# Optimization experiments

Hardware: AMD Instinct MI355X
Metric: run time of the kernel (lower is better)

Reference implementation:

```python
import jax, jax.numpy as jnp
import numpy as np

M, K, N, GROUP = 64, 4096, 11008, 128
NGROUPS = K // GROUP  # 32


def setup_inputs() -> dict:
    key = jax.random.key(0)
    k1, k2, k3, k4, k5 = jax.random.split(key, 5)
    x = jax.random.normal(k1, (M, K), dtype=jnp.float32)
    # packed int4 weights: 8 nibbles per int32, full 32-bit entropy
    qweight = jax.random.bits(k2, (K // 8, N), dtype=jnp.uint32).astype(jnp.int32)
    qzeros = jax.random.bits(k3, (NGROUPS, N // 8), dtype=jnp.uint32).astype(jnp.int32)
    scales = jax.random.uniform(k4, (NGROUPS, N), dtype=jnp.float32, minval=0.001, maxval=0.02)
    bias = jax.random.normal(k5, (N,), dtype=jnp.float32) * 0.01
    return {"x": x, "qweight": qweight, "qzeros": qzeros, "scales": scales, "bias": bias}


def dequantize(qweight, qzeros, scales):
    shifts = jnp.arange(8, dtype=jnp.int32) * 4  # nibble bit offsets 0..28
    # unpack weights: [K//8, N] -> [K//8, 8, N] -> [NGROUPS, GROUP, N]
    w = (jnp.right_shift(qweight[:, None, :], shifts[None, :, None]) & 15)
    w = w.reshape(-1, GROUP, qweight.shape[1])
    # unpack zeros: [NGROUPS, N//8] -> [NGROUPS, N//8, 8] -> [NGROUPS, 1, N]; GPTQ stores zero-1
    z = (jnp.right_shift(qzeros[:, :, None], shifts[None, None, :]) & 15) + 1
    z = z.reshape(z.shape[0], 1, -1)
    # scale * (q - zero), per group: [NGROUPS, GROUP, N] -> [K, N]
    W = scales[:, None, :] * (w - z).astype(scales.dtype)
    return W.reshape(-1, W.shape[2])


def reference(x, qweight, qzeros, scales, bias):
    W = dequantize(qweight, qzeros, scales)  # [K, N] fp32
    return jnp.matmul(x, W.astype(x.dtype)) + bias
```

## Files before the change

kernel.cpp:

```cpp
#include <hip/hip_runtime.h>
#include <hip/hip_bf16.h>

namespace {

constexpr int MM = 64;
constexpr int KK = 4096;
constexpr int NN = 11008;
constexpr int NZROW = NN / 8;
constexpr int BN = 128;
constexpr int KSPLIT = 8;
constexpr int KSEG = KK / KSPLIT;
constexpr int NTILES = NN / BN;
constexpr int SCK = 128;
constexpr int NSC = KSEG / SCK;
constexpr int AROW = 68;
constexpr int ABUF = MM * AROW;
constexpr size_t WS_NEED = (size_t)KSPLIT * MM * NN * 4;

typedef float f32x4 __attribute__((ext_vector_type(4)));
typedef short s16x8 __attribute__((ext_vector_type(8)));
typedef int   i32x4 __attribute__((ext_vector_type(4)));

__device__ __forceinline__ int perm_trunc(float even, float odd) {
  return (int)__builtin_amdgcn_perm(__float_as_uint(odd), __float_as_uint(even), 0x07060302u);
}
__device__ __forceinline__ unsigned rne_adj(float f) {
  unsigned u = __float_as_uint(f);
  return u + 0x7FFFu + ((u >> 16) & 1u);
}
__device__ __forceinline__ int pack_rne(float even, float odd) {
  return (int)__builtin_amdgcn_perm(rne_adj(odd), rne_adj(even), 0x07060302u);
}

__global__ __launch_bounds__(256) void prep_kernel(
    const float* __restrict__ bias, float* __restrict__ out)
{
  const int i = blockIdx.x * 256 + threadIdx.x;
  out[i] = bias[i % NN];
}

__global__ __launch_bounds__(256) void reduce_kernel(
    const float* __restrict__ ws, const float* __restrict__ bias,
    float* __restrict__ out)
{
  const int i4 = (blockIdx.x * 256 + threadIdx.x) * 4;
  f32x4 acc = *(const f32x4*)(bias + (i4 % NN));
  #pragma unroll
  for (int s = 0; s < KSPLIT; ++s)
    acc += *(const f32x4*)(ws + (size_t)s * (MM * NN) + i4);
  *(f32x4*)(out + i4) = acc;
}

template<bool ATOMIC>
__global__ __launch_bounds__(256, 3) void gptq_gemm_kernel(
    const float* __restrict__ x, const int* __restrict__ qw,
    const int* __restrict__ qz, const float* __restrict__ scales,
    float* __restrict__ out)
{
  __shared__ int Albuf[2 * ABUF];

  const int tid  = threadIdx.x;
  const int wave = tid >> 6;
  const int lane = tid & 63;
  const int c    = lane & 15;
  const int quad = lane >> 4;

  const int ks    = blockIdx.x & 7;
  const int ntile = blockIdx.x >> 3;
  const int n0    = ntile * BN;
  const int kbase = ks * KSEG;

  const int sm  = tid >> 2;
  const int skq = tid & 3;
  const float* xs = x + sm * KK + kbase + skq * 32;

  const int nb0   = n0 + wave * 32;
  const int ncol0 = nb0 + c;
  const int ncol1 = nb0 + 16 + c;
  const int* qwl  = qw + (size_t)quad * NN + ncol0;
  const int g0    = ks * NSC;

  f32x4 acc[8];
  #pragma unroll
  for (int i = 0; i < 8; ++i) acc[i] = {0.f, 0.f, 0.f, 0.f};

  f32x4 xv[8];
  int   qv[4][2];
  float ps0[2], ps1[2];
  int   pz0[2], pz1[2];

  auto stage = [&](int sl) {
    int* Ab = Albuf + sl * ABUF;
    int iw[16];
    #pragma unroll
    for (int j = 0; j < 8; ++j) {
      iw[2 * j]     = pack_rne(xv[j].x, xv[j].y);
      iw[2 * j + 1] = pack_rne(xv[j].z, xv[j].w);
    }
    #pragma unroll
    for (int gq = 0; gq < 4; ++gq)
      *(i32x4*)&Ab[sm * AROW + skq * 16 + gq * 4] = *(const i32x4*)&iw[gq * 4];
  };

  #pragma unroll
  for (int j = 0; j < 8; ++j) xv[j] = *(const f32x4*)(xs + j * 4);
  #pragma unroll
  for (int ch = 0; ch < 4; ++ch) {
    const size_t ro = (size_t)(ks * 64 + ch * 4) * NN;
    qv[ch][0] = qwl[ro];
    qv[ch][1] = qwl[ro + 16];
  }
  ps0[0] = scales[(size_t)g0 * NN + ncol0];
  ps1[0] = scales[(size_t)g0 * NN + ncol1];
  pz0[0] = qz[(size_t)g0 * NZROW + (ncol0 >> 3)];
  pz1[0] = qz[(size_t)g0 * NZROW + (ncol1 >> 3)];
  stage(0);
  __asm__ volatile("s_waitcnt lgkmcnt(0)\n\ts_barrier" ::: "memory");

  #pragma unroll
  for (int s = 0; s < NSC; ++s) {
    const int sl = s & 1;
    if (s + 1 < NSC) {
      #pragma unroll
      for (int j = 0; j < 8; ++j) xv[j] = *(const f32x4*)(xs + (s + 1) * SCK + j * 4);
      const int g1 = g0 + s + 1;
      ps0[(s + 1) & 1] = scales[(size_t)g1 * NN + ncol0];
      ps1[(s + 1) & 1] = scales[(size_t)g1 * NN + ncol1];
      pz0[(s + 1) & 1] = qz[(size_t)g1 * NZROW + (ncol0 >> 3)];
      pz1[(s + 1) & 1] = qz[(size_t)g1 * NZROW + (ncol1 >> 3)];
    }
    const float s0v = ps0[sl], s1v = ps1[sl];
    const float C0 = (float)(0x800000 + ((pz0[sl] >> ((ncol0 & 7) * 4)) & 15) + 1);
    const float C1 = (float)(0x800000 + ((pz1[sl] >> ((ncol1 & 7) * 4)) & 15) + 1);
    const int* Ab = Albuf + sl * ABUF;

    #pragma unroll
    for (int ch = 0; ch < 4; ++ch) {
      const int v0 = qv[ch][0], v1 = qv[ch][1];
      if (s + 1 < NSC) {
        const size_t ro = (size_t)(ks * 64 + (s + 1) * 16 + ch * 4) * NN;
        qv[ch][0] = qwl[ro];
        qv[ch][1] = qwl[ro + 16];
      }
      i32x4 b0, b1;
      {
        const float w0 = s0v * (__int_as_float(((v0      ) & 15) | 0x4B000000) - C0);
        const float w1 = s0v * (__int_as_float(((v0 >>  4) & 15) | 0x4B000000) - C0);
        const float w2 = s0v * (__int_as_float(((v0 >>  8) & 15) | 0x4B000000) - C0);
        const float w3 = s0v * (__int_as_float(((v0 >> 12) & 15) | 0x4B000000) - C0);
        const float w4 = s0v * (__int_as_float(((v0 >> 16) & 15) | 0x4B000000) - C0);
        const float w5 = s0v * (__int_as_float(((v0 >> 20) & 15) | 0x4B000000) - C0);
        const float w6 = s0v * (__int_as_float(((v0 >> 24) & 15) | 0x4B000000) - C0);
        const float w7 = s0v * (__int_as_float(((v0 >> 28) & 15) | 0x4B000000) - C0);
        b0.x = perm_trunc(w0, w1); b0.y = perm_trunc(w2, w3);
        b0.z = perm_trunc(w4, w5); b0.w = perm_trunc(w6, w7);
      }
      {
        const float w0 = s1v * (__int_as_float(((v1      ) & 15) | 0x4B000000) - C1);
        const float w1 = s1v * (__int_as_float(((v1 >>  4) & 15) | 0x4B000000) - C1);
        const float w2 = s1v * (__int_as_float(((v1 >>  8) & 15) | 0x4B000000) - C1);
        const float w3 = s1v * (__int_as_float(((v1 >> 12) & 15) | 0x4B000000) - C1);
        const float w4 = s1v * (__int_as_float(((v1 >> 16) & 15) | 0x4B000000) - C1);
        const float w5 = s1v * (__int_as_float(((v1 >> 20) & 15) | 0x4B000000) - C1);
        const float w6 = s1v * (__int_as_float(((v1 >> 24) & 15) | 0x4B000000) - C1);
        const float w7 = s1v * (__int_as_float(((v1 >> 28) & 15) | 0x4B000000) - C1);
        b1.x = perm_trunc(w0, w1); b1.y = perm_trunc(w2, w3);
        b1.z = perm_trunc(w4, w5); b1.w = perm_trunc(w6, w7);
      }
      const s16x8 bf0 = __builtin_bit_cast(s16x8, b0);
      const s16x8 bf1 = __builtin_bit_cast(s16x8, b1);

      #pragma unroll
      for (int t = 0; t < 4; ++t) {
        const s16x8 af = *(const s16x8*)&Ab[(16 * t + c) * AROW + ch * 16 + quad * 4];
        acc[2 * t]     = __builtin_amdgcn_mfma_f32_16x16x32_bf16(af, bf0, acc[2 * t],     0, 0, 0);
        acc[2 * t + 1] = __builtin_amdgcn_mfma_f32_16x16x32_bf16(af, bf1, acc[2 * t + 1], 0, 0, 0);
      }
    }

    if (s + 1 < NSC) {
      stage((s + 1) & 1);
      __asm__ volatile("s_waitcnt lgkmcnt(0)\n\ts_barrier" ::: "memory");
    }
  }

  if (ATOMIC) {
    #pragma unroll
    for (int t = 0; t < 4; ++t)
      #pragma unroll
      for (int u = 0; u < 2; ++u) {
        const int N = nb0 + u * 16 + c;
        const f32x4 a = acc[2 * t + u];
        const int m0 = 16 * t + quad * 4;
        atomicAdd(&out[(m0 + 0) * NN + N], a.x);
        atomicAdd(&out[(m0 + 1) * NN + N], a.y);
        atomicAdd(&out[(m0 + 2) * NN + N], a.z);
        atomicAdd(&out[(m0 + 3) * NN + N], a.w);
      }
  } else {
    float* wsp = out + (size_t)ks * (MM * NN);
    #pragma unroll
    for (int t = 0; t < 4; ++t)
      #pragma unroll
      for (int u = 0; u < 2; ++u) {
        const int N = nb0 + u * 16 + c;
        const f32x4 a = acc[2 * t + u];
        const int m0 = 16 * t + quad * 4;
        wsp[(m0 + 0) * NN + N] = a.x;
        wsp[(m0 + 1) * NN + N] = a.y;
        wsp[(m0 + 2) * NN + N] = a.z;
        wsp[(m0 + 3) * NN + N] = a.w;
      }
  }
}

}

extern "C" void kernel_launch(void* const* d_in, const int* in_sizes, int n_in,
                              void* d_out, int out_size, void* d_ws, size_t ws_size,
                              hipStream_t stream) {
  const float* x      = (const float*)d_in[0];
  const int*   qw     = (const int*)d_in[1];
  const int*   qz     = (const int*)d_in[2];
  const float* scales = (const float*)d_in[3];
  const float* bias   = (const float*)d_in[4];
  float* out = (float*)d_out;

  if (ws_size >= WS_NEED) {
    float* ws = (float*)d_ws;
    gptq_gemm_kernel<false><<<NTILES * KSPLIT, 256, 0, stream>>>(x, qw, qz, scales, ws);
    reduce_kernel<<<(MM * NN) / 1024, 256, 0, stream>>>(ws, bias, out);
  } else {
    prep_kernel<<<(MM * NN) / 256, 256, 0, stream>>>(bias, out);
    gptq_gemm_kernel<true><<<NTILES * KSPLIT, 256, 0, stream>>>(x, qw, qz, scales, out);
  }
}
```

Measured before the change: 98.03 us.

## Fuse split-K reduction into GEMM via per-tile counter and deepen qweight prefetch

Removes the separate reduce kernel. Each block now increments a per-N-tile atomic counter after writing its partial, and the last of the K-split blocks sums all partials plus bias into the output. Qweight loads are double-buffered two stages ahead instead of one, to hide more memory latency. This adds a memset launch, a threadfence and an atomic per block, and leaves a serialized tail reduction in the last block of each tile. The extra qweight buffer also raises register pressure.

```diff
diff --git a/kernel.cpp b/kernel.cpp
--- a/kernel.cpp
+++ b/kernel.cpp
@@ -15,7 +15,8 @@
 constexpr int NSC = KSEG / SCK;
 constexpr int AROW = 68;
 constexpr int ABUF = MM * AROW;
-constexpr size_t WS_NEED = (size_t)KSPLIT * MM * NN * 4;
+constexpr size_t CNT_OFF = (size_t)KSPLIT * MM * NN;
+constexpr size_t WS_NEED = CNT_OFF * 4 + NTILES * 4;
 
 typedef float f32x4 __attribute__((ext_vector_type(4)));
 typedef short s16x8 __attribute__((ext_vector_type(8)));
@@ -39,25 +40,15 @@
   out[i] = bias[i % NN];
 }
 
-__global__ __launch_bounds__(256) void reduce_kernel(
-    const float* __restrict__ ws, const float* __restrict__ bias,
-    float* __restrict__ out)
-{
-  const int i4 = (blockIdx.x * 256 + threadIdx.x) * 4;
-  f32x4 acc = *(const f32x4*)(bias + (i4 % NN));
-  #pragma unroll
-  for (int s = 0; s < KSPLIT; ++s)
-    acc += *(const f32x4*)(ws + (size_t)s * (MM * NN) + i4);
-  *(f32x4*)(out + i4) = acc;
-}
-
 template<bool ATOMIC>
 __global__ __launch_bounds__(256, 3) void gptq_gemm_kernel(
     const float* __restrict__ x, const int* __restrict__ qw,
     const int* __restrict__ qz, const float* __restrict__ scales,
-    float* __restrict__ out)
+    const float* __restrict__ bias, float* __restrict__ ws,
+    int* __restrict__ cnt, float* __restrict__ out)
 {
   __shared__ int Albuf[2 * ABUF];
+  __shared__ int last_flag;
 
   const int tid  = threadIdx.x;
   const int wave = tid >> 6;
@@ -85,7 +76,7 @@
   for (int i = 0; i < 8; ++i) acc[i] = {0.f, 0.f, 0.f, 0.f};
 
   f32x4 xv[8];
-  int   qv[4][2];
+  int   qv[2][4][2];
   float ps0[2], ps1[2];
   int   pz0[2], pz1[2];
 
@@ -101,15 +92,18 @@
     for (int gq = 0; gq < 4; ++gq)
       *(i32x4*)&Ab[sm * AROW + skq * 16 + gq * 4] = *(const i32x4*)&iw[gq * 4];
   };
-
+  auto pfQ = [&](int s) {
+    #pragma unroll
+    for (int ch = 0; ch < 4; ++ch) {
+      const size_t ro = (size_t)(ks * 64 + s * 16 + ch * 4) * NN;
+      qv[s & 1][ch][0] = qwl[ro];
+      qv[s & 1][ch][1] = qwl[ro + 16];
+    }
+  };
+
+  pfQ(0); pfQ(1);
   #pragma unroll
   for (int j = 0; j < 8; ++j) xv[j] = *(const f32x4*)(xs + j * 4);
-  #pragma unroll
-  for (int ch = 0; ch < 4; ++ch) {
-    const size_t ro = (size_t)(ks * 64 + ch * 4) * NN;
-    qv[ch][0] = qwl[ro];
-    qv[ch][1] = qwl[ro + 16];
-  }
   ps0[0] = scales[(size_t)g0 * NN + ncol0];
   ps1[0] = scales[(size_t)g0 * NN + ncol1];
   pz0[0] = qz[(size_t)g0 * NZROW + (ncol0 >> 3)];
@@ -136,11 +130,11 @@
 
     #pragma unroll
     for (int ch = 0; ch < 4; ++ch) {
-      const int v0 = qv[ch][0], v1 = qv[ch][1];
-      if (s + 1 < NSC) {
-        const size_t ro = (size_t)(ks * 64 + (s + 1) * 16 + ch * 4) * NN;
-        qv[ch][0] = qwl[ro];
-        qv[ch][1] = qwl[ro + 16];
+      const int v0 = qv[sl][ch][0], v1 = qv[sl][ch][1];
+      if (s + 2 < NSC) {
+        const size_t ro = (size_t)(ks * 64 + (s + 2) * 16 + ch * 4) * NN;
+        qv[sl][ch][0] = qwl[ro];
+        qv[sl][ch][1] = qwl[ro + 16];
       }
       i32x4 b0, b1;
       {
@@ -198,7 +192,7 @@
         atomicAdd(&out[(m0 + 3) * NN + N], a.w);
       }
   } else {
-    float* wsp = out + (size_t)ks * (MM * NN);
+    float* wsp = ws + (size_t)ks * (MM * NN);
     #pragma unroll
     for (int t = 0; t < 4; ++t)
       #pragma unroll
@@ -211,6 +205,28 @@
         wsp[(m0 + 2) * NN + N] = a.z;
         wsp[(m0 + 3) * NN + N] = a.w;
       }
+    __threadfence();
+    __syncthreads();
+    if (tid == 0) {
+      const int prev = __hip_atomic_fetch_add(&cnt[ntile], 1,
+                          __ATOMIC_ACQ_REL, __HIP_MEMORY_SCOPE_AGENT);
+      last_flag = (prev == KSPLIT - 1);
+    }
+    __syncthreads();
+    if (last_flag) {
+      #pragma unroll
+      for (int j = 0; j < 8; ++j) {
+        const int idx = j * 256 + tid;
+        const int m   = idx >> 5;
+        const int nc  = n0 + (idx & 31) * 4;
+        const size_t o = (size_t)m * NN + nc;
+        f32x4 sum = *(const f32x4*)(bias + nc);
+        #pragma unroll
+        for (int p = 0; p < KSPLIT; ++p)
+          sum += *(const f32x4*)(ws + (size_t)p * (MM * NN) + o);
+        *(f32x4*)(out + o) = sum;
+      }
+    }
   }
 }
 
@@ -227,11 +243,14 @@
   float* out = (float*)d_out;
 
   if (ws_size >= WS_NEED) {
-    float* ws = (float*)d_ws;
-    gptq_gemm_kernel<false><<<NTILES * KSPLIT, 256, 0, stream>>>(x, qw, qz, scales, ws);
-    reduce_kernel<<<(MM * NN) / 1024, 256, 0, stream>>>(ws, bias, out);
+    float* ws  = (float*)d_ws;
+    int*   cnt = (int*)(ws + CNT_OFF);
+    hipMemsetAsync(cnt, 0, NTILES * sizeof(int), stream);
+    gptq_gemm_kernel<false><<<NTILES * KSPLIT, 256, 0, stream>>>(
+        x, qw, qz, scales, bias, ws, cnt, out);
   } else {
     prep_kernel<<<(MM * NN) / 256, 256, 0, stream>>>(bias, out);
-    gptq_gemm_kernel<true><<<NTILES * KSPLIT, 256, 0, stream>>>(x, qw, qz, scales, out);
+    gptq_gemm_kernel<true><<<NTILES * KSPLIT, 256, 0, stream>>>(
+        x, qw, qz, scales, bias, nullptr, nullptr, out);
   }
 }
```

New measurement: 218.9 us. +123.3%, slower.

## Pre-convert x to bf16 fragment layout and drop LDS staging in GEMM

Applied to the files above, without the earlier changes.

Adds a pre-pass kernel that converts x to bf16 and writes it in the MFMA fragment layout, so the GEMM loads B fragments straight from global/L2 with no LDS staging and no barriers. Dequantized weights become the A operand, scales and zeros are hoisted for all groups, and qweight is prefetched two steps ahead. Each block writes its partial tile contiguously in fragment order, and the reduce kernel is rewritten to gather that layout. This trades an extra launch plus repeated global loads of the small x tensor for removing LDS traffic and synchronization.

```diff
diff --git a/kernel.cpp b/kernel.cpp
--- a/kernel.cpp
+++ b/kernel.cpp
@@ -7,15 +7,13 @@
 constexpr int KK = 4096;
 constexpr int NN = 11008;
 constexpr int NZROW = NN / 8;
-constexpr int BN = 128;
 constexpr int KSPLIT = 8;
 constexpr int KSEG = KK / KSPLIT;
-constexpr int NTILES = NN / BN;
-constexpr int SCK = 128;
-constexpr int NSC = KSEG / SCK;
-constexpr int AROW = 68;
-constexpr int ABUF = MM * AROW;
-constexpr size_t WS_NEED = (size_t)KSPLIT * MM * NN * 4;
+constexpr int NTILES = NN / 128;
+constexpr int NCH = KSEG / 32;
+constexpr int BLK_FLOATS = 64 * 128;
+constexpr size_t XT8_OFF = (size_t)NTILES * KSPLIT * BLK_FLOATS;
+constexpr size_t WS_NEED = XT8_OFF * 4 + (size_t)KK * MM * 2;
 
 typedef float f32x4 __attribute__((ext_vector_type(4)));
 typedef short s16x8 __attribute__((ext_vector_type(8)));
@@ -32,6 +30,25 @@
   return (int)__builtin_amdgcn_perm(rne_adj(odd), rne_adj(even), 0x07060302u);
 }
 
+__device__ short g_xT8[KK * MM];
+
+__global__ __launch_bounds__(256) void xt8_kernel(
+    const float* __restrict__ x, short* __restrict__ xT8)
+{
+  if (xT8 == nullptr) xT8 = g_xT8;
+  const int m    = blockIdx.x >> 1;
+  const int kblk = (blockIdx.x & 1) * 256 + threadIdx.x;
+  const float* p = x + m * KK + kblk * 8;
+  const f32x4 a = *(const f32x4*)p;
+  const f32x4 b = *(const f32x4*)(p + 4);
+  i32x4 w;
+  w.x = pack_rne(a.x, a.y);
+  w.y = pack_rne(a.z, a.w);
+  w.z = pack_rne(b.x, b.y);
+  w.w = pack_rne(b.z, b.w);
+  *(i32x4*)(xT8 + ((size_t)kblk * MM + m) * 8) = w;
+}
+
 __global__ __launch_bounds__(256) void prep_kernel(
     const float* __restrict__ bias, float* __restrict__ out)
 {
@@ -44,173 +61,150 @@
     float* __restrict__ out)
 {
   const int i4 = (blockIdx.x * 256 + threadIdx.x) * 4;
-  f32x4 acc = *(const f32x4*)(bias + (i4 % NN));
-  #pragma unroll
-  for (int s = 0; s < KSPLIT; ++s)
-    acc += *(const f32x4*)(ws + (size_t)s * (MM * NN) + i4);
-  *(f32x4*)(out + i4) = acc;
+  const int m  = i4 / NN;
+  const int n  = i4 - m * NN;
+  const int ntile = n >> 7, nt = n & 127;
+  const int wv = nt >> 5, ns = (nt >> 4) & 1, qd = (nt >> 2) & 3;
+  const int mt = m >> 4,  ml = m & 15;
+  const float* base = ws + (size_t)(ntile * 8) * BLK_FLOATS
+                    + ((wv * 8 + ns * 4 + mt) * 64 + qd * 16 + ml) * 4;
+  f32x4 sum = *(const f32x4*)(bias + n);
+  #pragma unroll
+  for (int p = 0; p < KSPLIT; ++p)
+    sum += *(const f32x4*)(base + (size_t)p * BLK_FLOATS);
+  *(f32x4*)(out + i4) = sum;
 }
 
 template<bool ATOMIC>
 __global__ __launch_bounds__(256, 3) void gptq_gemm_kernel(
-    const float* __restrict__ x, const int* __restrict__ qw,
-    const int* __restrict__ qz, const float* __restrict__ scales,
-    float* __restrict__ out)
-{
-  __shared__ int Albuf[2 * ABUF];
-
+    const int* __restrict__ qw, const int* __restrict__ qz,
+    const float* __restrict__ scales, const short* __restrict__ xT8p,
+    float* __restrict__ outws)
+{
+  const short* xT8 = (xT8p == nullptr) ? g_xT8 : xT8p;
   const int tid  = threadIdx.x;
   const int wave = tid >> 6;
   const int lane = tid & 63;
-  const int c    = lane & 15;
+  const int ml   = lane & 15;
   const int quad = lane >> 4;
 
   const int ks    = blockIdx.x & 7;
   const int ntile = blockIdx.x >> 3;
-  const int n0    = ntile * BN;
-  const int kbase = ks * KSEG;
-
-  const int sm  = tid >> 2;
-  const int skq = tid & 3;
-  const float* xs = x + sm * KK + kbase + skq * 32;
-
-  const int nb0   = n0 + wave * 32;
-  const int ncol0 = nb0 + c;
-  const int ncol1 = nb0 + 16 + c;
-  const int* qwl  = qw + (size_t)quad * NN + ncol0;
-  const int g0    = ks * NSC;
-
-  f32x4 acc[8];
-  #pragma unroll
-  for (int i = 0; i < 8; ++i) acc[i] = {0.f, 0.f, 0.f, 0.f};
-
-  f32x4 xv[8];
-  int   qv[4][2];
-  float ps0[2], ps1[2];
-  int   pz0[2], pz1[2];
-
-  auto stage = [&](int sl) {
-    int* Ab = Albuf + sl * ABUF;
-    int iw[16];
-    #pragma unroll
-    for (int j = 0; j < 8; ++j) {
-      iw[2 * j]     = pack_rne(xv[j].x, xv[j].y);
-      iw[2 * j + 1] = pack_rne(xv[j].z, xv[j].w);
-    }
-    #pragma unroll
-    for (int gq = 0; gq < 4; ++gq)
-      *(i32x4*)&Ab[sm * AROW + skq * 16 + gq * 4] = *(const i32x4*)&iw[gq * 4];
-  };
-
-  #pragma unroll
-  for (int j = 0; j < 8; ++j) xv[j] = *(const f32x4*)(xs + j * 4);
-  #pragma unroll
-  for (int ch = 0; ch < 4; ++ch) {
-    const size_t ro = (size_t)(ks * 64 + ch * 4) * NN;
-    qv[ch][0] = qwl[ro];
-    qv[ch][1] = qwl[ro + 16];
-  }
-  ps0[0] = scales[(size_t)g0 * NN + ncol0];
-  ps1[0] = scales[(size_t)g0 * NN + ncol1];
-  pz0[0] = qz[(size_t)g0 * NZROW + (ncol0 >> 3)];
-  pz1[0] = qz[(size_t)g0 * NZROW + (ncol1 >> 3)];
-  stage(0);
-  __asm__ volatile("s_waitcnt lgkmcnt(0)\n\ts_barrier" ::: "memory");
-
-  #pragma unroll
-  for (int s = 0; s < NSC; ++s) {
+  const int nw0   = ntile * 128 + wave * 32;
+  const int ncol0 = nw0 + ml;
+  const int rbase = ks * 64;
+
+  const int* qwl = qw + (size_t)(rbase + quad) * NN + ncol0;
+
+  const int g0 = ks * 4;
+  float s0[4], s1[4], C0[4], C1[4];
+  #pragma unroll
+  for (int s = 0; s < 4; ++s) {
+    s0[s] = scales[(size_t)(g0 + s) * NN + ncol0];
+    s1[s] = scales[(size_t)(g0 + s) * NN + ncol0 + 16];
+    const int z0 = (qz[(size_t)(g0 + s) * NZROW + ((ncol0)      >> 3)] >> ((ncol0 & 7) * 4)) & 15;
+    const int z1 = (qz[(size_t)(g0 + s) * NZROW + ((ncol0 + 16) >> 3)] >> ((ncol0 & 7) * 4)) & 15;
+    C0[s] = (float)(0x800000 + z0 + 1);
+    C1[s] = (float)(0x800000 + z1 + 1);
+  }
+
+  int qv[2][4][2];
+  #pragma unroll
+  for (int s = 0; s < 2; ++s)
+    #pragma unroll
+    for (int ch = 0; ch < 4; ++ch) {
+      const size_t ro = (size_t)(s * 16 + ch * 4) * NN;
+      qv[s][ch][0] = qwl[ro];
+      qv[s][ch][1] = qwl[ro + 16];
+    }
+
+  const s16x8* xb = (const s16x8*)xT8;
+  const int bbase = (rbase + quad) * MM + ml;
+  s16x8 bf[2][4];
+  #pragma unroll
+  for (int mt = 0; mt < 4; ++mt) bf[0][mt] = xb[bbase + mt * 16];
+
+  f32x4 acc[2][4];
+  #pragma unroll
+  for (int a = 0; a < 2; ++a)
+    #pragma unroll
+    for (int b = 0; b < 4; ++b) acc[a][b] = {0.f, 0.f, 0.f, 0.f};
+
+  #pragma unroll
+  for (int g = 0; g < NCH; ++g) {
+    const int s  = g >> 2;
+    const int ch = g & 3;
     const int sl = s & 1;
-    if (s + 1 < NSC) {
+
+    if (g + 1 < NCH) {
       #pragma unroll
-      for (int j = 0; j < 8; ++j) xv[j] = *(const f32x4*)(xs + (s + 1) * SCK + j * 4);
-      const int g1 = g0 + s + 1;
-      ps0[(s + 1) & 1] = scales[(size_t)g1 * NN + ncol0];
-      ps1[(s + 1) & 1] = scales[(size_t)g1 * NN + ncol1];
-      pz0[(s + 1) & 1] = qz[(size_t)g1 * NZROW + (ncol0 >> 3)];
-      pz1[(s + 1) & 1] = qz[(size_t)g1 * NZROW + (ncol1 >> 3)];
-    }
-    const float s0v = ps0[sl], s1v = ps1[sl];
-    const float C0 = (float)(0x800000 + ((pz0[sl] >> ((ncol0 & 7) * 4)) & 15) + 1);
-    const float C1 = (float)(0x800000 + ((pz1[sl] >> ((ncol1 & 7) * 4)) & 15) + 1);
-    const int* Ab = Albuf + sl * ABUF;
-
-    #pragma unroll
-    for (int ch = 0; ch < 4; ++ch) {
-      const int v0 = qv[ch][0], v1 = qv[ch][1];
-      if (s + 1 < NSC) {
-        const size_t ro = (size_t)(ks * 64 + (s + 1) * 16 + ch * 4) * NN;
-        qv[ch][0] = qwl[ro];
-        qv[ch][1] = qwl[ro + 16];
-      }
-      i32x4 b0, b1;
-      {
-        const float w0 = s0v * (__int_as_float(((v0      ) & 15) | 0x4B000000) - C0);
-        const float w1 = s0v * (__int_as_float(((v0 >>  4) & 15) | 0x4B000000) - C0);
-        const float w2 = s0v * (__int_as_float(((v0 >>  8) & 15) | 0x4B000000) - C0);
-        const float w3 = s0v * (__int_as_float(((v0 >> 12) & 15) | 0x4B000000) - C0);
-        const float w4 = s0v * (__int_as_float(((v0 >> 16) & 15) | 0x4B000000) - C0);
-        const float w5 = s0v * (__int_as_float(((v0 >> 20) & 15) | 0x4B000000) - C0);
-        const float w6 = s0v * (__int_as_float(((v0 >> 24) & 15) | 0x4B000000) - C0);
-        const float w7 = s0v * (__int_as_float(((v0 >> 28) & 15) | 0x4B000000) - C0);
-        b0.x = perm_trunc(w0, w1); b0.y = perm_trunc(w2, w3);
-        b0.z = perm_trunc(w4, w5); b0.w = perm_trunc(w6, w7);
-      }
-      {
-        const float w0 = s1v * (__int_as_float(((v1      ) & 15) | 0x4B000000) - C1);
-        const float w1 = s1v * (__int_as_float(((v1 >>  4) & 15) | 0x4B000000) - C1);
-        const float w2 = s1v * (__int_as_float(((v1 >>  8) & 15) | 0x4B000000) - C1);
-        const float w3 = s1v * (__int_as_float(((v1 >> 12) & 15) | 0x4B000000) - C1);
-        const float w4 = s1v * (__int_as_float(((v1 >> 16) & 15) | 0x4B000000) - C1);
-        const float w5 = s1v * (__int_as_float(((v1 >> 20) & 15) | 0x4B000000) - C1);
-        const float w6 = s1v * (__int_as_float(((v1 >> 24) & 15) | 0x4B000000) - C1);
-        const float w7 = s1v * (__int_as_float(((v1 >> 28) & 15) | 0x4B000000) - C1);
-        b1.x = perm_trunc(w0, w1); b1.y = perm_trunc(w2, w3);
-        b1.z = perm_trunc(w4, w5); b1.w = perm_trunc(w6, w7);
-      }
-      const s16x8 bf0 = __builtin_bit_cast(s16x8, b0);
-      const s16x8 bf1 = __builtin_bit_cast(s16x8, b1);
-
+      for (int mt = 0; mt < 4; ++mt)
+        bf[(g + 1) & 1][mt] = xb[bbase + (g + 1) * 4 * MM + mt * 16];
+    }
+
+    const int v0 = qv[sl][ch][0], v1 = qv[sl][ch][1];
+    if (s + 2 < 4) {
+      const size_t ro = (size_t)((s + 2) * 16 + ch * 4) * NN;
+      qv[sl][ch][0] = qwl[ro];
+      qv[sl][ch][1] = qwl[ro + 16];
+    }
+
+    const float sa = s0[s], sb = s1[s], Ca = C0[s], Cb = C1[s];
+    i32x4 b0, b1;
+    {
+      const float w0 = sa * (__int_as_float(((v0      ) & 15) | 0x4B000000) - Ca);
+      const float w1 = sa * (__int_as_float(((v0 >>  4) & 15) | 0x4B000000) - Ca);
+      const float w2 = sa * (__int_as_float(((v0 >>  8) & 15) | 0x4B000000) - Ca);
+      const float w3 = sa * (__int_as_float(((v0 >> 12) & 15) | 0x4B000000) - Ca);
+      const float w4 = sa * (__int_as_float(((v0 >> 16) & 15) | 0x4B000000) - Ca);
+      const float w5 = sa * (__int_as_float(((v0 >> 20) & 15) | 0x4B000000) - Ca);
+      const float w6 = sa * (__int_as_float(((v0 >> 24) & 15) | 0x4B000000) - Ca);
+      const float w7 = sa * (__int_as_float(((v0 >> 28) & 15) | 0x4B000000) - Ca);
+      b0.x = perm_trunc(w0, w1); b0.y = perm_trunc(w2, w3);
+      b0.z = perm_trunc(w4, w5); b0.w = perm_trunc(w6, w7);
+    }
+    {
+      const float w0 = sb * (__int_as_float(((v1      ) & 15) | 0x4B000000) - Cb);
+      const float w1 = sb * (__int_as_float(((v1 >>  4) & 15) | 0x4B000000) - Cb);
+      const float w2 = sb * (__int_as_float(((v1 >>  8) & 15) | 0x4B000000) - Cb);
+      const float w3 = sb * (__int_as_float(((v1 >> 12) & 15) | 0x4B000000) - Cb);
+      const float w4 = sb * (__int_as_float(((v1 >> 16) & 15) | 0x4B000000) - Cb);
+      const float w5 = sb * (__int_as_float(((v1 >> 20) & 15) | 0x4B000000) - Cb);
+      const float w6 = sb * (__int_as_float(((v1 >> 24) & 15) | 0x4B000000) - Cb);
+      const float w7 = sb * (__int_as_float(((v1 >> 28) & 15) | 0x4B000000) - Cb);
+      b1.x = perm_trunc(w0, w1); b1.y = perm_trunc(w2, w3);
+      b1.z = perm_trunc(w4, w5); b1.w = perm_trunc(w6, w7);
+    }
+    const s16x8 wf0 = __builtin_bit_cast(s16x8, b0);
+    const s16x8 wf1 = __builtin_bit_cast(s16x8, b1);
+
+    #pragma unroll
+    for (int mt = 0; mt < 4; ++mt) {
+      acc[0][mt] = __builtin_amdgcn_mfma_f32_16x16x32_bf16(wf0, bf[g & 1][mt], acc[0][mt], 0, 0, 0);
+      acc[1][mt] = __builtin_amdgcn_mfma_f32_16x16x32_bf16(wf1, bf[g & 1][mt], acc[1][mt], 0, 0, 0);
+    }
+  }
+
+  if (ATOMIC) {
+    #pragma unroll
+    for (int ns = 0; ns < 2; ++ns)
       #pragma unroll
-      for (int t = 0; t < 4; ++t) {
-        const s16x8 af = *(const s16x8*)&Ab[(16 * t + c) * AROW + ch * 16 + quad * 4];
-        acc[2 * t]     = __builtin_amdgcn_mfma_f32_16x16x32_bf16(af, bf0, acc[2 * t],     0, 0, 0);
-        acc[2 * t + 1] = __builtin_amdgcn_mfma_f32_16x16x32_bf16(af, bf1, acc[2 * t + 1], 0, 0, 0);
-      }
-    }
-
-    if (s + 1 < NSC) {
-      stage((s + 1) & 1);
-      __asm__ volatile("s_waitcnt lgkmcnt(0)\n\ts_barrier" ::: "memory");
-    }
-  }
-
-  if (ATOMIC) {
-    #pragma unroll
-    for (int t = 0; t < 4; ++t)
-      #pragma unroll
-      for (int u = 0; u < 2; ++u) {
-        const int N = nb0 + u * 16 + c;
-        const f32x4 a = acc[2 * t + u];
-        const int m0 = 16 * t + quad * 4;
-        atomicAdd(&out[(m0 + 0) * NN + N], a.x);
-        atomicAdd(&out[(m0 + 1) * NN + N], a.y);
-        atomicAdd(&out[(m0 + 2) * NN + N], a.z);
-        atomicAdd(&out[(m0 + 3) * NN + N], a.w);
+      for (int mt = 0; mt < 4; ++mt) {
+        const int m = mt * 16 + ml;
+        const int nb = nw0 + ns * 16 + quad * 4;
+        const f32x4 a = acc[ns][mt];
+        atomicAdd(&outws[(size_t)m * NN + nb + 0], a.x);
+        atomicAdd(&outws[(size_t)m * NN + nb + 1], a.y);
+        atomicAdd(&outws[(size_t)m * NN + nb + 2], a.z);
+        atomicAdd(&outws[(size_t)m * NN + nb + 3], a.w);
       }
   } else {
-    float* wsp = out + (size_t)ks * (MM * NN);
-    #pragma unroll
-    for (int t = 0; t < 4; ++t)
+    float* wsb = outws + (size_t)blockIdx.x * BLK_FLOATS;
+    #pragma unroll
+    for (int ns = 0; ns < 2; ++ns)
       #pragma unroll
-      for (int u = 0; u < 2; ++u) {
-        const int N = nb0 + u * 16 + c;
-        const f32x4 a = acc[2 * t + u];
-        const int m0 = 16 * t + quad * 4;
-        wsp[(m0 + 0) * NN + N] = a.x;
-        wsp[(m0 + 1) * NN + N] = a.y;
-        wsp[(m0 + 2) * NN + N] = a.z;
-        wsp[(m0 + 3) * NN + N] = a.w;
-      }
+      for (int mt = 0; mt < 4; ++mt)
+        *(f32x4*)(wsb + ((wave * 8 + ns * 4 + mt) * 64 + lane) * 4) = acc[ns][mt];
   }
 }
 
@@ -227,11 +221,14 @@
   float* out = (float*)d_out;
 
   if (ws_size >= WS_NEED) {
-    float* ws = (float*)d_ws;
-    gptq_gemm_kernel<false><<<NTILES * KSPLIT, 256, 0, stream>>>(x, qw, qz, scales, ws);
+    float* ws   = (float*)d_ws;
+    short* xT8  = (short*)(ws + XT8_OFF);
+    xt8_kernel<<<2 * MM, 256, 0, stream>>>(x, xT8);
+    gptq_gemm_kernel<false><<<NTILES * KSPLIT, 256, 0, stream>>>(qw, qz, scales, xT8, ws);
     reduce_kernel<<<(MM * NN) / 1024, 256, 0, stream>>>(ws, bias, out);
   } else {
+    xt8_kernel<<<2 * MM, 256, 0, stream>>>(x, nullptr);
     prep_kernel<<<(MM * NN) / 256, 256, 0, stream>>>(bias, out);
-    gptq_gemm_kernel<true><<<NTILES * KSPLIT, 256, 0, stream>>>(x, qw, qz, scales, out);
-  }
-}
+    gptq_gemm_kernel<true><<<NTILES * KSPLIT, 256, 0, stream>>>(qw, qz, scales, nullptr, out);
+  }
+}
```

Result: slower. 107.4 us (+9.6%).
